# Kernel tuning notes

Hardware: AMD Instinct MI355X
Metric: run time of the kernel (lower is better)

## Reference

```python
import jax, jax.numpy as jnp
import numpy as np

EPS = 1e-6
H, A, V = 4, 64, 64  # heads, attn_dim, hidden_dim


def layer_norm(x, w, b):
    mu = jnp.mean(x, axis=-1, keepdims=True)
    var = jnp.var(x, axis=-1, keepdims=True)
    return (x - mu) * jax.lax.rsqrt(var + EPS) * w + b


def setup_inputs() -> dict:
    key = jax.random.key(0)
    B, N, D = 4, 2048, 512
    lengths = np.array([2048, 1536, 1024, 1792], np.int32)
    offsets = np.concatenate([[0], np.cumsum(lengths)]).astype(np.int32)
    L = int(offsets[-1])  # 6400
    uvqk_out = (2 * V + 2 * A) * H  # 1024
    out_in = 2 * V * H + D          # concat([u, x, normed_attn])
    ks = jax.random.split(key, 4)
    return {
        "x": jax.random.normal(ks[0], (L, D), jnp.float32),
        "x_lengths": jnp.asarray(lengths),
        "x_offsets": jnp.asarray(offsets),
        "max_seq_len": N,
        "num_targets": jnp.asarray([32, 16, 8, 64], jnp.int32),
        "uvqk_weight": jax.random.normal(ks[1], (D, uvqk_out), jnp.float32) / np.float32(np.sqrt(D)),
        "uvqk_bias": jnp.zeros((uvqk_out,), jnp.float32),
        "input_norm_weight": jnp.ones((D,), jnp.float32),
        "input_norm_bias": jnp.zeros((D,), jnp.float32),
        "output_norm_weight": jnp.ones((V * H,), jnp.float32),
        "output_norm_bias": jnp.zeros((V * H,), jnp.float32),
        "output_weight": jax.random.normal(ks[2], (out_in, D), jnp.float32) / np.float32(np.sqrt(out_in)),
    }


def reference(x, x_lengths, x_offsets, max_seq_len, num_targets,
              uvqk_weight, uvqk_bias, input_norm_weight, input_norm_bias,
              output_norm_weight, output_norm_bias, output_weight):
    L, D = x.shape
    B = x_lengths.shape[0]
    N = int(max_seq_len)
    alpha = A ** -0.5

    # fused input layernorm + UVQK projection + silu
    nx = layer_norm(x, input_norm_weight, input_norm_bias)
    uvqk = jax.nn.silu(nx @ uvqk_weight + uvqk_bias)              # [L, (2V+2A)*H]
    u = uvqk[:, : V * H]                                          # [L, V*H]
    v = uvqk[:, V * H: 2 * V * H].reshape(L, H, V)
    q = uvqk[:, 2 * V * H: 2 * V * H + A * H].reshape(L, H, A)
    k = uvqk[:, 2 * V * H + A * H:].reshape(L, H, A)

    # jagged -> padded [B, N, ...]
    pos = jnp.arange(N)
    gather_idx = jnp.clip(x_offsets[:-1, None] + pos[None, :], 0, L - 1)  # [B,N]
    valid = pos[None, :] < x_lengths[:, None]                              # [B,N]
    qp = q[gather_idx] * valid[..., None, None]
    kp = k[gather_idx] * valid[..., None, None]
    vp = v[gather_idx] * valid[..., None, None]

    # target-aware causal mask: clamp ids at uih boundary; eye | dist>0
    max_ids = (x_lengths - num_targets)[:, None]        # [B,1]
    ids = jnp.minimum(pos[None, :], max_ids)            # [B,N]
    dist = ids[:, :, None] - ids[:, None, :]            # [B,N,N]
    mask = (dist > 0) | jnp.eye(N, dtype=bool)[None]
    mask = mask & valid[:, :, None] & valid[:, None, :]

    scores = jnp.einsum("bnha,bmha->bhnm", qp, kp) * alpha
    attn_w = jax.nn.silu(scores) * (1.0 / N)
    attn_w = attn_w * mask[:, None].astype(attn_w.dtype)
    attn_p = jnp.einsum("bhnm,bmhv->bnhv", attn_w, vp).reshape(B, N, H * V)

    # padded -> jagged
    tok = jnp.arange(L)
    b_of = jnp.searchsorted(x_offsets, tok, side="right") - 1
    p_of = tok - x_offsets[b_of]
    attn = attn_p[b_of, p_of]                            # [L, H*V]

    # output: norm(attn), concat [u, x, y], project, residual (dropout off / eval)
    y = layer_norm(attn, output_norm_weight, output_norm_bias)
    y = jnp.concatenate([u, x, y], axis=1)
    return x + y @ output_weight
```

## Files before the change

### kernel.cpp

```cpp
#include <hip/hip_runtime.h>
#include <math.h>

#define NSEQ 2048
#define PIT 72

typedef __attribute__((ext_vector_type(8))) short short8;
typedef __attribute__((ext_vector_type(4))) short short4v;
typedef __attribute__((ext_vector_type(4))) float f32x4;

__device__ __forceinline__ float silu_f(float z) {
    return z * __builtin_amdgcn_rcpf(1.f + __expf(-z));
}

__device__ __forceinline__ unsigned short f2bf(float f) {
    unsigned int u = __float_as_uint(f);
    u += 0x7fffu + ((u >> 16) & 1u);
    return (unsigned short)(u >> 16);
}

__device__ __forceinline__ unsigned short f2bf_fast(float f) {
    return (unsigned short)((__float_as_uint(f) + 0x8000u) >> 16);
}

__device__ __forceinline__ short8 scale8_pow2(short8 v, float s) {
    short8 r;
    #pragma unroll
    for (int i = 0; i < 8; i++) {
        float f = __uint_as_float(((unsigned int)(unsigned short)v[i]) << 16) * s;
        r[i] = (short)(unsigned short)(__float_as_uint(f) >> 16);
    }
    return r;
}

__device__ __forceinline__ void gload16(const unsigned short* g, unsigned short* l) {
    __builtin_amdgcn_global_load_lds(
        (const __attribute__((address_space(1))) unsigned short*)g,
        (__attribute__((address_space(3))) unsigned short*)l, 16, 0, 0);
}

__global__ void __launch_bounds__(256) prep_kernel(
    const float* __restrict__ W1, unsigned short* __restrict__ W1t,
    const float* __restrict__ W2, unsigned short* __restrict__ W2t,
    const float* __restrict__ x, const float* __restrict__ inw,
    const float* __restrict__ inb,
    unsigned short* __restrict__ nxb, unsigned short* __restrict__ A2)
{
    __shared__ float t[32][33];
    int id = blockIdx.x;
    int tid = threadIdx.x;
    if (id < 1024) {
        const float* W; unsigned short* Wt; int R, C, bx, by;
        if (id < 512) { W = W1; Wt = W1t; R = 512;  C = 1024; bx = id & 31; by = id >> 5; }
        else { int i2 = id - 512; W = W2; Wt = W2t; R = 1024; C = 512; bx = i2 & 15; by = i2 >> 4; }
        int r0 = by * 32, c0 = bx * 32;
        int rr = tid >> 3, cc = (tid & 7) * 4;
        float4 v = *(const float4*)(W + (size_t)(r0 + rr) * C + c0 + cc);
        t[rr][cc] = v.x; t[rr][cc + 1] = v.y; t[rr][cc + 2] = v.z; t[rr][cc + 3] = v.w;
        __syncthreads();
        int tr = tid >> 5, tc = tid & 31;
        #pragma unroll
        for (int p = 0; p < 4; p++)
            Wt[(size_t)(c0 + tr + p * 8) * R + r0 + tc] = f2bf(t[tc][tr + p * 8]);
        return;
    }
    int lane = tid & 63, wv = tid >> 6;
    int row = (id - 1024) * 4 + wv;
    int c = lane * 8;
    const float* xr = x + (size_t)row * 512 + c;
    float4 v0 = *(const float4*)xr;
    float4 v1 = *(const float4*)(xr + 4);
    float s  = v0.x + v0.y + v0.z + v0.w + v1.x + v1.y + v1.z + v1.w;
    float sq = v0.x * v0.x + v0.y * v0.y + v0.z * v0.z + v0.w * v0.w
             + v1.x * v1.x + v1.y * v1.y + v1.z * v1.z + v1.w * v1.w;
    #pragma unroll
    for (int o = 32; o > 0; o >>= 1) { s += __shfl_xor(s, o); sq += __shfl_xor(sq, o); }
    float mu = s * (1.f / 512.f);
    float var = sq * (1.f / 512.f) - mu * mu;
    float rs = rsqrtf(var + 1e-6f);
    float4 w0 = *(const float4*)(inw + c), w1 = *(const float4*)(inw + c + 4);
    float4 b0 = *(const float4*)(inb + c), b1 = *(const float4*)(inb + c + 4);
    ushort4 hn0, hn1, hx0, hx1;
    hn0.x = f2bf((v0.x - mu) * rs * w0.x + b0.x);
    hn0.y = f2bf((v0.y - mu) * rs * w0.y + b0.y);
    hn0.z = f2bf((v0.z - mu) * rs * w0.z + b0.z);
    hn0.w = f2bf((v0.w - mu) * rs * w0.w + b0.w);
    hn1.x = f2bf((v1.x - mu) * rs * w1.x + b1.x);
    hn1.y = f2bf((v1.y - mu) * rs * w1.y + b1.y);
    hn1.z = f2bf((v1.z - mu) * rs * w1.z + b1.z);
    hn1.w = f2bf((v1.w - mu) * rs * w1.w + b1.w);
    hx0.x = f2bf(v0.x); hx0.y = f2bf(v0.y); hx0.z = f2bf(v0.z); hx0.w = f2bf(v0.w);
    hx1.x = f2bf(v1.x); hx1.y = f2bf(v1.y); hx1.z = f2bf(v1.z); hx1.w = f2bf(v1.w);
    unsigned short* nr = nxb + (size_t)row * 512 + c;
    *(ushort4*)nr = hn0; *(ushort4*)(nr + 4) = hn1;
    unsigned short* ar = A2 + (size_t)row * 1024 + 256 + c;
    *(ushort4*)ar = hx0; *(ushort4*)(ar + 4) = hx1;
}

__global__ void __launch_bounds__(256) ln256_kernel(
    const float* __restrict__ a, const float* __restrict__ w,
    const float* __restrict__ b, unsigned short* __restrict__ A2)
{
    int tid = threadIdx.x, lane = tid & 63, wv = tid >> 6;
    int row = blockIdx.x * 4 + wv;
    int c = lane * 4;
    float4 v = *(const float4*)(a + (size_t)row * 256 + c);
    float s  = v.x + v.y + v.z + v.w;
    float sq = v.x * v.x + v.y * v.y + v.z * v.z + v.w * v.w;
    #pragma unroll
    for (int o = 32; o > 0; o >>= 1) { s += __shfl_xor(s, o); sq += __shfl_xor(sq, o); }
    float mu = s * (1.f / 256.f);
    float var = sq * (1.f / 256.f) - mu * mu;
    float rs = rsqrtf(var + 1e-6f);
    float4 w4 = *(const float4*)(w + c);
    float4 b4 = *(const float4*)(b + c);
    ushort4 h;
    h.x = f2bf((v.x - mu) * rs * w4.x + b4.x);
    h.y = f2bf((v.y - mu) * rs * w4.y + b4.y);
    h.z = f2bf((v.z - mu) * rs * w4.z + b4.z);
    h.w = f2bf((v.w - mu) * rs * w4.w + b4.w);
    *(ushort4*)(A2 + (size_t)row * 1024 + 768 + c) = h;
}


__global__ void __launch_bounds__(256, 5) gemm1_mfma(
    const unsigned short* __restrict__ Ab, const unsigned short* __restrict__ Bt,
    const float* __restrict__ bias,
    unsigned short* __restrict__ A2, unsigned short* __restrict__ qkvb)
{
    constexpr int K = 512, KIT = 8;
    __shared__ unsigned short lds[16384];
    int p = blockIdx.x;
    int l = (p & 7) * 200 + (p >> 3);
    int bm = (l >> 4) * 64, bn = (l & 15) * 64;
    int tid = threadIdx.x, lane = tid & 63, w = tid >> 6;
    int wr = w >> 1, wc = w & 1;
    int nn = lane & 15, qd = lane >> 4;

    int r8 = lane >> 3, u = lane & 7;
    int su = ((u ^ r8) << 3);
    int rA0 = w * 16;
    const unsigned short* Asrc = Ab + (size_t)(bm + rA0 + r8) * K + su;
    const unsigned short* Bsrc = Bt + (size_t)(bn + rA0 + r8) * K + su;

    int fsw = nn & 7;

    f32x4 acc[2][2];
    #pragma unroll
    for (int i = 0; i < 2; i++)
        #pragma unroll
        for (int j = 0; j < 2; j++) acc[i][j] = (f32x4){0.f, 0.f, 0.f, 0.f};

    gload16(Asrc,              &lds[rA0 * 64]);
    gload16(Asrc + 8 * K,      &lds[(rA0 + 8) * 64]);
    gload16(Bsrc,              &lds[4096 + rA0 * 64]);
    gload16(Bsrc + 8 * K,      &lds[4096 + (rA0 + 8) * 64]);
    gload16(Asrc + 64,         &lds[8192 + rA0 * 64]);
    gload16(Asrc + 8 * K + 64, &lds[8192 + (rA0 + 8) * 64]);
    gload16(Bsrc + 64,         &lds[12288 + rA0 * 64]);
    gload16(Bsrc + 8 * K + 64, &lds[12288 + (rA0 + 8) * 64]);

    for (int it = 0; it < KIT; ++it) {
        int cur = it & 1;
        unsigned short* Asc = lds + cur * 8192;
        unsigned short* Bsc = Asc + 4096;
        if (it == KIT - 1) asm volatile("s_waitcnt vmcnt(0)" ::: "memory");
        else               asm volatile("s_waitcnt vmcnt(4)" ::: "memory");
        __builtin_amdgcn_s_barrier();
        #pragma unroll
        for (int kk = 0; kk < 2; kk++) {
            int un = (((kk * 4 + qd) ^ fsw) << 3);
            short8 af[2], bf[2];
            #pragma unroll
            for (int i = 0; i < 2; i++)
                af[i] = *(const short8*)&Asc[(wr * 32 + i * 16 + nn) * 64 + un];
            #pragma unroll
            for (int j = 0; j < 2; j++)
                bf[j] = *(const short8*)&Bsc[(wc * 32 + j * 16 + nn) * 64 + un];
            #pragma unroll
            for (int i = 0; i < 2; i++)
                #pragma unroll
                for (int j = 0; j < 2; j++)
                    acc[i][j] = __builtin_amdgcn_mfma_f32_16x16x32_bf16(af[i], bf[j], acc[i][j], 0, 0, 0);
        }
        __builtin_amdgcn_s_barrier();
        if (it + 2 < KIT) {
            const unsigned short* a2 = Asrc + (it + 2) * 64;
            const unsigned short* b2 = Bsrc + (it + 2) * 64;
            gload16(a2,         &Asc[rA0 * 64]);
            gload16(a2 + 8 * K, &Asc[(rA0 + 8) * 64]);
            gload16(b2,         &Bsc[rA0 * 64]);
            gload16(b2 + 8 * K, &Bsc[(rA0 + 8) * 64]);
        }
    }

    bool isU = (bn < 256);
    #pragma unroll
    for (int j = 0; j < 2; j++) {
        int col = bn + wc * 32 + j * 16 + nn;
        float bb = bias[col];
        #pragma unroll
        for (int i = 0; i < 2; i++) {
            int rbase = bm + wr * 32 + i * 16 + qd * 4;
            #pragma unroll
            for (int r = 0; r < 4; r++) {
                unsigned short hh = f2bf(silu_f(acc[i][j][r] + bb));
                if (isU) A2[(size_t)(rbase + r) * 1024 + col] = hh;
                else     qkvb[(size_t)(rbase + r) * 768 + col - 256] = hh;
            }
        }
    }
}

__global__ void __launch_bounds__(256, 5) gemm2_mfma(
    const unsigned short* __restrict__ Ab, const unsigned short* __restrict__ Bt,
    const float* __restrict__ x, float* __restrict__ out)
{
    constexpr int K = 1024, KIT = 16;
    __shared__ unsigned short lds[16384];
    int p = blockIdx.x;
    int l = (p & 7) * 100 + (p >> 3);
    int bm = (l >> 3) * 64, bn = (l & 7) * 64;
    int tid = threadIdx.x, lane = tid & 63, w = tid >> 6;
    int wr = w >> 1, wc = w & 1;
    int nn = lane & 15, qd = lane >> 4;

    int r8 = lane >> 3, u = lane & 7;
    int su = ((u ^ r8) << 3);
    int rA0 = w * 16;
    const unsigned short* Asrc = Ab + (size_t)(bm + rA0 + r8) * K + su;
    const unsigned short* Bsrc = Bt + (size_t)(bn + rA0 + r8) * K + su;

    int fsw = nn & 7;

    f32x4 acc[2][2];
    #pragma unroll
    for (int i = 0; i < 2; i++)
        #pragma unroll
        for (int j = 0; j < 2; j++) acc[i][j] = (f32x4){0.f, 0.f, 0.f, 0.f};

    gload16(Asrc,              &lds[rA0 * 64]);
    gload16(Asrc + 8 * K,      &lds[(rA0 + 8) * 64]);
    gload16(Bsrc,              &lds[4096 + rA0 * 64]);
    gload16(Bsrc + 8 * K,      &lds[4096 + (rA0 + 8) * 64]);
    gload16(Asrc + 64,         &lds[8192 + rA0 * 64]);
    gload16(Asrc + 8 * K + 64, &lds[8192 + (rA0 + 8) * 64]);
    gload16(Bsrc + 64,         &lds[12288 + rA0 * 64]);
    gload16(Bsrc + 8 * K + 64, &lds[12288 + (rA0 + 8) * 64]);

    for (int it = 0; it < KIT; ++it) {
        int cur = it & 1;
        unsigned short* Asc = lds + cur * 8192;
        unsigned short* Bsc = Asc + 4096;
        if (it == KIT - 1) asm volatile("s_waitcnt vmcnt(0)" ::: "memory");
        else               asm volatile("s_waitcnt vmcnt(4)" ::: "memory");
        __builtin_amdgcn_s_barrier();
        #pragma unroll
        for (int kk = 0; kk < 2; kk++) {
            int un = (((kk * 4 + qd) ^ fsw) << 3);
            short8 af[2], bf[2];
            #pragma unroll
            for (int i = 0; i < 2; i++)
                af[i] = *(const short8*)&Asc[(wr * 32 + i * 16 + nn) * 64 + un];
            #pragma unroll
            for (int j = 0; j < 2; j++)
                bf[j] = *(const short8*)&Bsc[(wc * 32 + j * 16 + nn) * 64 + un];
            #pragma unroll
            for (int i = 0; i < 2; i++)
                #pragma unroll
                for (int j = 0; j < 2; j++)
                    acc[i][j] = __builtin_amdgcn_mfma_f32_16x16x32_bf16(af[i], bf[j], acc[i][j], 0, 0, 0);
        }
        __builtin_amdgcn_s_barrier();
        if (it + 2 < KIT) {
            const unsigned short* a2 = Asrc + (it + 2) * 64;
            const unsigned short* b2 = Bsrc + (it + 2) * 64;
            gload16(a2,         &Asc[rA0 * 64]);
            gload16(a2 + 8 * K, &Asc[(rA0 + 8) * 64]);
            gload16(b2,         &Bsc[rA0 * 64]);
            gload16(b2 + 8 * K, &Bsc[(rA0 + 8) * 64]);
        }
    }

    #pragma unroll
    for (int j = 0; j < 2; j++) {
        int col = bn + wc * 32 + j * 16 + nn;
        #pragma unroll
        for (int i = 0; i < 2; i++) {
            int rbase = bm + wr * 32 + i * 16 + qd * 4;
            #pragma unroll
            for (int r = 0; r < 4; r++) {
                size_t idx = (size_t)(rbase + r) * 512 + col;
                out[idx] = x[idx] + acc[i][j][r];
            }
        }
    }
}

__global__ void __launch_bounds__(256, 2) attn_mfma_kernel(
    const unsigned short* __restrict__ qkvb,
    const int* __restrict__ offsets,
    const int* __restrict__ lengths,
    const int* __restrict__ num_targets,
    float* __restrict__ attn)
{
    int id = blockIdx.x;
    int bh = id & 15;
    int xt = id >> 4;
    int b = bh >> 2, h = bh & 3;
    int len = lengths[b];
    int n0 = (31 - xt) * 64;
    if (n0 >= len) return;
    int m_hi = min(n0 + 63, len - 1);
    int off = offsets[b];
    int max_id = len - num_targets[b];
    int tid = threadIdx.x, lane = tid & 63, w = tid >> 6;
    int nn = lane & 15, qd = lane >> 4;

    __shared__ __align__(16) char smem[69632];
    unsigned short* Vt = (unsigned short*)(smem + w * 9216);
    float* Os = (float*)smem;

    short8 qf[4][2];
    #pragma unroll
    for (int g = 0; g < 4; g++) {
        int row = min(n0 + g * 16 + nn, len - 1);
        const unsigned short* base = qkvb + (size_t)(off + row) * 768 + 256 + h * 64;
        qf[g][0] = scale8_pow2(*(const short8*)(base + qd * 8), 0.125f);
        qf[g][1] = scale8_pow2(*(const short8*)(base + 32 + qd * 8), 0.125f);
    }

    f32x4 o_acc[4][4];
    #pragma unroll
    for (int t = 0; t < 4; t++)
        #pragma unroll
        for (int g = 0; g < 4; g++) o_acc[t][g] = (f32x4){0.f, 0.f, 0.f, 0.f};

    int fast_lim = min(n0, max_id);
    int r0 = (lane & 15) * 4, d0 = (lane >> 4) * 16;

    short8 kf[4][2], kn[4][2], vf[4][2];
    int m_first = w * 64;
    if (m_first <= m_hi) {
        #pragma unroll
        for (int s = 0; s < 4; s++) {
            int row = min(m_first + s * 16 + nn, len - 1);
            const unsigned short* kb = qkvb + (size_t)(off + row) * 768 + 512 + h * 64 + qd * 8;
            kf[s][0] = *(const short8*)kb;
            kf[s][1] = *(const short8*)(kb + 32);
        }
        #pragma unroll
        for (int j = 0; j < 4; j++) {
            int row = min(m_first + r0 + j, len - 1);
            const unsigned short* vb = qkvb + (size_t)(off + row) * 768 + h * 64 + d0;
            vf[j][0] = *(const short8*)vb;
            vf[j][1] = *(const short8*)(vb + 8);
        }
    }

    for (int m0 = m_first; m0 <= m_hi; m0 += 256) {
        #pragma unroll
        for (int dd = 0; dd < 16; dd++) {
            int hh = dd >> 3, e = dd & 7;
            short4v pk;
            pk[0] = vf[0][hh][e]; pk[1] = vf[1][hh][e];
            pk[2] = vf[2][hh][e]; pk[3] = vf[3][hh][e];
            *(short4v*)&Vt[(d0 + dd) * PIT + r0] = pk;
        }
        int mnext = m0 + 256;
        if (mnext <= m_hi) {
            #pragma unroll
            for (int j = 0; j < 4; j++) {
                int row = min(mnext + r0 + j, len - 1);
                const unsigned short* vb = qkvb + (size_t)(off + row) * 768 + h * 64 + d0;
                vf[j][0] = *(const short8*)vb;
                vf[j][1] = *(const short8*)(vb + 8);
            }
            #pragma unroll
            for (int s = 0; s < 4; s++) {
                int row = min(mnext + s * 16 + nn, len - 1);
                const unsigned short* kb = qkvb + (size_t)(off + row) * 768 + 512 + h * 64 + qd * 8;
                kn[s][0] = *(const short8*)kb;
                kn[s][1] = *(const short8*)(kb + 32);
            }
        }
        bool fastp = (m0 + 63 < fast_lim);
        #pragma unroll
        for (int s = 0; s < 4; s++) {
            f32x4 st[4];
            __builtin_amdgcn_s_setprio(1);
            #pragma unroll
            for (int g = 0; g < 4; g++) {
                st[g] = (f32x4){0.f, 0.f, 0.f, 0.f};
                st[g] = __builtin_amdgcn_mfma_f32_16x16x32_bf16(kf[s][0], qf[g][0], st[g], 0, 0, 0);
                st[g] = __builtin_amdgcn_mfma_f32_16x16x32_bf16(kf[s][1], qf[g][1], st[g], 0, 0, 0);
            }
            __builtin_amdgcn_s_setprio(0);
            short4v bop[4];
            if (fastp) {
                #pragma unroll
                for (int g = 0; g < 4; g++)
                    #pragma unroll
                    for (int r = 0; r < 4; r++)
                        bop[g][r] = (short)f2bf_fast(silu_f(st[g][r]));
            } else {
                #pragma unroll
                for (int g = 0; g < 4; g++) {
                    int nc_ = n0 + g * 16 + nn;
                    int id_ = min(nc_, max_id);
                    #pragma unroll
                    for (int r = 0; r < 4; r++) {
                        int mcol = m0 + s * 16 + qd * 4 + r;
                        bool ok = (mcol < id_) || (mcol == nc_);
                        bop[g][r] = (short)f2bf_fast(ok ? silu_f(st[g][r]) : 0.f);
                    }
                }
            }
            __builtin_amdgcn_s_setprio(1);
            #pragma unroll
            for (int t = 0; t < 4; t++) {
                short4v aop = *(const short4v*)&Vt[(t * 16 + nn) * PIT + s * 16 + qd * 4];
                #pragma unroll
                for (int g = 0; g < 4; g++)
                    o_acc[t][g] = __builtin_amdgcn_mfma_f32_16x16x16bf16_1k(aop, bop[g], o_acc[t][g], 0, 0, 0);
            }
            __builtin_amdgcn_s_setprio(0);
        }
        if (mnext <= m_hi) {
            #pragma unroll
            for (int s = 0; s < 4; s++) { kf[s][0] = kn[s][0]; kf[s][1] = kn[s][1]; }
        }
    }

    __syncthreads();
    const float invN = 1.f / (float)NSEQ;
    float* Ow = Os + w * 4352;
    #pragma unroll
    for (int t = 0; t < 4; t++)
        #pragma unroll
        for (int g = 0; g < 4; g++) {
            f32x4 v = o_acc[t][g] * invN;
            *(f32x4*)&Ow[(g * 16 + nn) * 68 + t * 16 + qd * 4] = v;
        }
    __syncthreads();
    int rr = tid >> 2, cs = (tid & 3) * 16;
    if (n0 + rr < len) {
        float* dst = attn + (size_t)(off + n0 + rr) * 256 + h * 64 + cs;
        #pragma unroll
        for (int q4 = 0; q4 < 4; q4++) {
            f32x4 v = (f32x4){0.f, 0.f, 0.f, 0.f};
            #pragma unroll
            for (int w2 = 0; w2 < 4; w2++)
                v += *(const f32x4*)&Os[w2 * 4352 + rr * 68 + cs + q4 * 4];
            *(f32x4*)(dst + q4 * 4) = v;
        }
    }
}

extern "C" void kernel_launch(void* const* d_in, const int* in_sizes, int n_in,
                              void* d_out, int out_size, void* d_ws, size_t ws_size,
                              hipStream_t stream)
{
    const float* x          = (const float*)d_in[0];
    const int*   x_lengths  = (const int*)d_in[1];
    const int*   x_offsets  = (const int*)d_in[2];
    const int*   num_targets = (const int*)d_in[4];
    const float* uvqk_w     = (const float*)d_in[5];
    const float* uvqk_b     = (const float*)d_in[6];
    const float* in_w       = (const float*)d_in[7];
    const float* in_b       = (const float*)d_in[8];
    const float* out_w      = (const float*)d_in[9];
    const float* out_b      = (const float*)d_in[10];
    const float* Wo         = (const float*)d_in[11];
    float* out = (float*)d_out;

    int L = in_sizes[0] / 512;

    char* ws = (char*)d_ws;
    size_t o = 0;
    float* attn = (float*)(ws + o);          o += (size_t)L * 256 * 4;
    unsigned short* nxb  = (unsigned short*)(ws + o); o += (size_t)L * 512 * 2;
    unsigned short* A2   = (unsigned short*)(ws + o); o += (size_t)L * 1024 * 2;
    unsigned short* qkvb = (unsigned short*)(ws + o); o += (size_t)L * 768 * 2;
    unsigned short* W1t  = (unsigned short*)(ws + o); o += (size_t)1024 * 512 * 2;
    unsigned short* W2t  = (unsigned short*)(ws + o); o += (size_t)512 * 1024 * 2;

    prep_kernel<<<dim3(1024 + L / 4), 256, 0, stream>>>(
        uvqk_w, W1t, Wo, W2t, x, in_w, in_b, nxb, A2);

    gemm1_mfma<<<dim3(1600), 256, 0, stream>>>(nxb, W1t, uvqk_b, A2, qkvb);

    attn_mfma_kernel<<<dim3(512), 256, 0, stream>>>(qkvb, x_offsets, x_lengths, num_targets, attn);

    ln256_kernel<<<L / 4, 256, 0, stream>>>(attn, out_w, out_b, A2);

    gemm2_mfma<<<dim3(800), 256, 0, stream>>>(A2, W2t, x, out);
}
```

Baseline: 150.7 us.

## Fuse output layernorm into attention kernel via last-block ticket counter

Removes the separate ln256 kernel launch. Each attention block bumps an atomic ticket for its (batch, row-tile), and the fourth head block to finish runs the 256-wide layernorm for those 64 rows and writes bf16 into A2. The prep kernel resets the tickets. This saves one launch and its gap, at the cost of a threadfence, an atomic and a serialized LN tail in the last block of each tile.

```diff
diff --git a/kernel.cpp b/kernel.cpp
--- a/kernel.cpp
+++ b/kernel.cpp
@@ -43,7 +43,8 @@
     const float* __restrict__ W2, unsigned short* __restrict__ W2t,
     const float* __restrict__ x, const float* __restrict__ inw,
     const float* __restrict__ inb,
-    unsigned short* __restrict__ nxb, unsigned short* __restrict__ A2)
+    unsigned short* __restrict__ nxb, unsigned short* __restrict__ A2,
+    int* __restrict__ tickets)
 {
     __shared__ float t[32][33];
     int id = blockIdx.x;
@@ -63,6 +64,7 @@
             Wt[(size_t)(c0 + tr + p * 8) * R + r0 + tc] = f2bf(t[tc][tr + p * 8]);
         return;
     }
+    if (id == 1024 && tid < 128) tickets[tid] = 0;
     int lane = tid & 63, wv = tid >> 6;
     int row = (id - 1024) * 4 + wv;
     int c = lane * 8;
@@ -96,31 +98,6 @@
     *(ushort4*)ar = hx0; *(ushort4*)(ar + 4) = hx1;
 }
 
-__global__ void __launch_bounds__(256) ln256_kernel(
-    const float* __restrict__ a, const float* __restrict__ w,
-    const float* __restrict__ b, unsigned short* __restrict__ A2)
-{
-    int tid = threadIdx.x, lane = tid & 63, wv = tid >> 6;
-    int row = blockIdx.x * 4 + wv;
-    int c = lane * 4;
-    float4 v = *(const float4*)(a + (size_t)row * 256 + c);
-    float s  = v.x + v.y + v.z + v.w;
-    float sq = v.x * v.x + v.y * v.y + v.z * v.z + v.w * v.w;
-    #pragma unroll
-    for (int o = 32; o > 0; o >>= 1) { s += __shfl_xor(s, o); sq += __shfl_xor(sq, o); }
-    float mu = s * (1.f / 256.f);
-    float var = sq * (1.f / 256.f) - mu * mu;
-    float rs = rsqrtf(var + 1e-6f);
-    float4 w4 = *(const float4*)(w + c);
-    float4 b4 = *(const float4*)(b + c);
-    ushort4 h;
-    h.x = f2bf((v.x - mu) * rs * w4.x + b4.x);
-    h.y = f2bf((v.y - mu) * rs * w4.y + b4.y);
-    h.z = f2bf((v.z - mu) * rs * w4.z + b4.z);
-    h.w = f2bf((v.w - mu) * rs * w4.w + b4.w);
-    *(ushort4*)(A2 + (size_t)row * 1024 + 768 + c) = h;
-}
-
 
 __global__ void __launch_bounds__(256, 5) gemm1_mfma(
     const unsigned short* __restrict__ Ab, const unsigned short* __restrict__ Bt,
@@ -301,7 +278,9 @@
     const int* __restrict__ offsets,
     const int* __restrict__ lengths,
     const int* __restrict__ num_targets,
-    float* __restrict__ attn)
+    float* __restrict__ attn,
+    const float* __restrict__ ow, const float* __restrict__ ob,
+    unsigned short* __restrict__ A2, int* __restrict__ tickets)
 {
     int id = blockIdx.x;
     int bh = id & 15;
@@ -317,6 +296,7 @@
     int nn = lane & 15, qd = lane >> 4;
 
     __shared__ __align__(16) char smem[69632];
+    __shared__ int lastflag;
     unsigned short* Vt = (unsigned short*)(smem + w * 9216);
     float* Os = (float*)smem;
 
@@ -454,6 +434,39 @@
             *(f32x4*)(dst + q4 * 4) = v;
         }
     }
+
+    __threadfence();
+    __syncthreads();
+    if (tid == 0) {
+        int old = __hip_atomic_fetch_add(&tickets[b * 32 + xt], 1,
+                                         __ATOMIC_ACQ_REL, __HIP_MEMORY_SCOPE_AGENT);
+        lastflag = (old == 3);
+    }
+    __syncthreads();
+    if (lastflag) {
+        int wv2 = tid >> 6, ln = tid & 63;
+        int c = ln * 4;
+        float4 w4 = *(const float4*)(ow + c);
+        float4 b4 = *(const float4*)(ob + c);
+        for (int r2 = wv2; r2 < 64; r2 += 4) {
+            if (n0 + r2 >= len) break;
+            size_t grow = (size_t)(off + n0 + r2);
+            float4 vx = *(const float4*)(attn + grow * 256 + c);
+            float s  = vx.x + vx.y + vx.z + vx.w;
+            float sq = vx.x * vx.x + vx.y * vx.y + vx.z * vx.z + vx.w * vx.w;
+            #pragma unroll
+            for (int o = 32; o > 0; o >>= 1) { s += __shfl_xor(s, o); sq += __shfl_xor(sq, o); }
+            float mu = s * (1.f / 256.f);
+            float var = sq * (1.f / 256.f) - mu * mu;
+            float rs = rsqrtf(var + 1e-6f);
+            ushort4 hy;
+            hy.x = f2bf((vx.x - mu) * rs * w4.x + b4.x);
+            hy.y = f2bf((vx.y - mu) * rs * w4.y + b4.y);
+            hy.z = f2bf((vx.z - mu) * rs * w4.z + b4.z);
+            hy.w = f2bf((vx.w - mu) * rs * w4.w + b4.w);
+            *(ushort4*)(A2 + grow * 1024 + 768 + c) = hy;
+        }
+    }
 }
 
 extern "C" void kernel_launch(void* const* d_in, const int* in_sizes, int n_in,
@@ -483,15 +496,15 @@
     unsigned short* qkvb = (unsigned short*)(ws + o); o += (size_t)L * 768 * 2;
     unsigned short* W1t  = (unsigned short*)(ws + o); o += (size_t)1024 * 512 * 2;
     unsigned short* W2t  = (unsigned short*)(ws + o); o += (size_t)512 * 1024 * 2;
+    int* tickets = (int*)(ws + o);           o += 128 * 4;
 
     prep_kernel<<<dim3(1024 + L / 4), 256, 0, stream>>>(
-        uvqk_w, W1t, Wo, W2t, x, in_w, in_b, nxb, A2);
+        uvqk_w, W1t, Wo, W2t, x, in_w, in_b, nxb, A2, tickets);
 
     gemm1_mfma<<<dim3(1600), 256, 0, stream>>>(nxb, W1t, uvqk_b, A2, qkvb);
 
-    attn_mfma_kernel<<<dim3(512), 256, 0, stream>>>(qkvb, x_offsets, x_lengths, num_targets, attn);
-
-    ln256_kernel<<<L / 4, 256, 0, stream>>>(attn, out_w, out_b, A2);
+    attn_mfma_kernel<<<dim3(512), 256, 0, stream>>>(
+        qkvb, x_offsets, x_lengths, num_targets, attn, out_w, out_b, A2, tickets);
 
     gemm2_mfma<<<dim3(800), 256, 0, stream>>>(A2, W2t, x, out);
 }
```

After: 219.0 us. +45.3%, slower.
